# Performance work log

Measured on AMD Instinct MI355X. Metric: run time of the kernel, lower is better.

The kernel has to match this reference:

```python
import jax, jax.numpy as jnp
import numpy as np

B, Q, O = 64, 16, 20   # batch, max questions, max objects
NUM_CAT = 101
D = 256                # category_embedding_dim
T = 4096               # max dialogue length (max_dln)


def setup_inputs() -> dict:
    key = jax.random.key(0)
    k1, k2, k3, k4, k5 = jax.random.split(key, 5)
    object_logits = jax.random.normal(k1, (B, Q, O), dtype=jnp.float32)
    emb_table = jax.random.normal(k2, (NUM_CAT, D), dtype=jnp.float32) * 0.05
    object_categories = jax.random.randint(k3, (B, O), 0, NUM_CAT)
    # sorted, positive cumulative token offsets per (batch, question)
    cumulative_lengths = jnp.sort(jax.random.randint(k4, (B, Q), 1, T + 1), axis=1)
    num_questions = jax.random.randint(k5, (B,), 2, Q + 1)
    return {
        "object_logits": object_logits,
        "emb_table": emb_table,
        "object_categories": object_categories,
        "cumulative_lengths": cumulative_lengths,
        "num_questions": num_questions,
        "max_dln": T,
    }


def reference(object_logits, emb_table, object_categories, cumulative_lengths,
              num_questions, max_dln):
    # --- belief state: softmax -> bmm -> tanh (fused) ---
    probs = jax.nn.softmax(object_logits, axis=-1)          # [B,Q,O]
    obj_emb = emb_table[object_categories]                  # [B,O,D]
    belief = jnp.tanh(jnp.einsum('bqo,bod->bqd', probs, obj_emb))  # [B,Q,D]

    b, q, _ = object_logits.shape
    t = jnp.arange(max_dln)                                 # [T]

    # Ranges in the original loop are contiguous:
    #   qi=0: [0, cum[:,1]-1), qi>=1: [cum[:,qi]-1, cum[:,qi+1]-1)
    # so boundary for question qi's end is cum[:, qi+1]-1 (j = qi+1 in 1..Q-1),
    # valid only for j <= num_questions-1. Mask padded boundaries to +inf.
    j = jnp.arange(1, q)                                    # [Q-1]
    bnd = jnp.where(j[None, :] <= num_questions[:, None] - 1,
                    cumulative_lengths[:, 1:] - 1,
                    max_dln + 1)                            # [B,Q-1]
    # question index owning token t = number of boundaries <= t
    qi = jnp.sum(t[None, None, :] >= bnd[:, :, None], axis=1)  # [B,T] int
    valid = qi < (num_questions[:, None] - 1)               # [B,T]

    qi_c = jnp.minimum(qi, q - 1)
    feats = jnp.take_along_axis(belief, qi_c[:, :, None], axis=1)  # [B,T,D]
    additional_features = jnp.where(valid[:, :, None], feats, 0.0)
    return additional_features
```

## Files before the change

kernel.cpp:

```cpp
#include <hip/hip_runtime.h>
#include <hip/hip_bf16.h>
#include <math.h>

constexpr int B_ = 64;
constexpr int Q_ = 16;
constexpr int O_ = 20;
constexpr int D_ = 256;

__global__ __launch_bounds__(D_) void belief_kernel(
    const float* __restrict__ logits,
    const float* __restrict__ emb,
    const int*   __restrict__ cats,
    float*       __restrict__ belief)
{
    const int bq = blockIdx.x;
    const int b  = bq >> 4;
    const int d  = threadIdx.x;

    __shared__ float s_logit[O_];
    __shared__ int   s_cat[O_];
    if (d < O_) {
        s_logit[d] = logits[bq * O_ + d];
        s_cat[d]   = cats[b * O_ + d];
    }
    __syncthreads();

    float m = -INFINITY;
    #pragma unroll
    for (int o = 0; o < O_; ++o) m = fmaxf(m, s_logit[o]);
    float w[O_];
    float sum = 0.f;
    #pragma unroll
    for (int o = 0; o < O_; ++o) { w[o] = expf(s_logit[o] - m); sum += w[o]; }
    const float inv = 1.f / sum;

    float acc = 0.f;
    #pragma unroll
    for (int o = 0; o < O_; ++o)
        acc = fmaf(w[o] * inv, emb[s_cat[o] * D_ + d], acc);

    belief[bq * D_ + d] = tanhf(acc);
}

constexpr int ROWS_ = 256;

__global__ __launch_bounds__(256) void expand_kernel(
    const float* __restrict__ belief,
    const int*   __restrict__ cum,
    const int*   __restrict__ nq_arr,
    float*       __restrict__ out,
    int T)
{
    const int b   = blockIdx.y;
    const int t0  = blockIdx.x * ROWS_;
    const int tid = threadIdx.x;

    __shared__ float s_belief[Q_ * D_];

    {
        const float4* src = (const float4*)(belief + (size_t)b * Q_ * D_);
        float4*       dst = (float4*)s_belief;
        #pragma unroll
        for (int i = 0; i < (Q_ * D_ / 4) / 256; ++i)
            dst[tid + i * 256] = src[tid + i * 256];
    }

    const int nq = nq_arr[b];
    int bnd[Q_ - 1];
    #pragma unroll
    for (int j = 1; j < Q_; ++j)
        bnd[j - 1] = (j <= nq - 1) ? (cum[b * Q_ + j] - 1) : 0x7fffffff;

    __syncthreads();

    const int col  = (tid & 63) * 4;
    const int rsub = tid >> 6;

    #pragma unroll 4
    for (int it = 0; it < ROWS_ / 4; ++it) {
        const int t = t0 + it * 4 + rsub;
        if (t >= T) break;

        int qi = 0;
        #pragma unroll
        for (int j = 0; j < Q_ - 1; ++j) qi += (t >= bnd[j]) ? 1 : 0;

        float4 v = make_float4(0.f, 0.f, 0.f, 0.f);
        if (qi < nq - 1) {
            const int qc = qi < (Q_ - 1) ? qi : (Q_ - 1);
            v = *(const float4*)(s_belief + qc * D_ + col);
        }
        *(float4*)(out + ((size_t)b * T + t) * (size_t)D_ + col) = v;
    }
}

extern "C" void kernel_launch(void* const* d_in, const int* in_sizes, int n_in,
                              void* d_out, int out_size, void* d_ws, size_t ws_size,
                              hipStream_t stream)
{
    const float* logits = (const float*)d_in[0];
    const float* emb    = (const float*)d_in[1];
    const int*   cats   = (const int*)d_in[2];
    const int*   cum    = (const int*)d_in[3];
    const int*   nq     = (const int*)d_in[4];

    float* out    = (float*)d_out;
    float* belief = (float*)d_ws;

    const int T = out_size / (B_ * D_);

    belief_kernel<<<B_ * Q_, D_, 0, stream>>>(logits, emb, cats, belief);

    dim3 grid((T + ROWS_ - 1) / ROWS_, B_);
    expand_kernel<<<grid, 256, 0, stream>>>(belief, cum, nq, out, T);
}
```

Measured before the change: 270.9 us.

## Fuse belief computation into expand kernel, recomputing per block

Folds the softmax-bmm-tanh belief computation into the expand kernel so each block computes its batch's 16x256 belief tile directly into shared memory. This drops the separate kernel launch and the workspace round trip through global memory. In exchange, every one of the 16 blocks per batch redundantly recomputes the same belief tile, with each thread producing 16 outputs using float4 embedding loads.

```diff
diff --git a/kernel.cpp b/kernel.cpp
--- a/kernel.cpp
+++ b/kernel.cpp
@@ -1,5 +1,4 @@
 #include <hip/hip_runtime.h>
-#include <hip/hip_bf16.h>
 #include <math.h>
 
 constexpr int B_ = 64;
@@ -7,45 +6,12 @@
 constexpr int O_ = 20;
 constexpr int D_ = 256;
 
-__global__ __launch_bounds__(D_) void belief_kernel(
+constexpr int ROWS_ = 256;
+
+__global__ __launch_bounds__(256) void fused_kernel(
     const float* __restrict__ logits,
     const float* __restrict__ emb,
     const int*   __restrict__ cats,
-    float*       __restrict__ belief)
-{
-    const int bq = blockIdx.x;
-    const int b  = bq >> 4;
-    const int d  = threadIdx.x;
-
-    __shared__ float s_logit[O_];
-    __shared__ int   s_cat[O_];
-    if (d < O_) {
-        s_logit[d] = logits[bq * O_ + d];
-        s_cat[d]   = cats[b * O_ + d];
-    }
-    __syncthreads();
-
-    float m = -INFINITY;
-    #pragma unroll
-    for (int o = 0; o < O_; ++o) m = fmaxf(m, s_logit[o]);
-    float w[O_];
-    float sum = 0.f;
-    #pragma unroll
-    for (int o = 0; o < O_; ++o) { w[o] = expf(s_logit[o] - m); sum += w[o]; }
-    const float inv = 1.f / sum;
-
-    float acc = 0.f;
-    #pragma unroll
-    for (int o = 0; o < O_; ++o)
-        acc = fmaf(w[o] * inv, emb[s_cat[o] * D_ + d], acc);
-
-    belief[bq * D_ + d] = tanhf(acc);
-}
-
-constexpr int ROWS_ = 256;
-
-__global__ __launch_bounds__(256) void expand_kernel(
-    const float* __restrict__ belief,
     const int*   __restrict__ cum,
     const int*   __restrict__ nq_arr,
     float*       __restrict__ out,
@@ -56,13 +22,51 @@
     const int tid = threadIdx.x;
 
     __shared__ float s_belief[Q_ * D_];
+    __shared__ float s_logit[Q_ * O_];
+    __shared__ int   s_cat[O_];
+
+    for (int i = tid; i < Q_ * O_; i += 256) s_logit[i] = logits[b * Q_ * O_ + i];
+    if (tid < O_) s_cat[tid] = cats[b * O_ + tid];
+    __syncthreads();
 
     {
-        const float4* src = (const float4*)(belief + (size_t)b * Q_ * D_);
-        float4*       dst = (float4*)s_belief;
+        const int q  = tid >> 4;
+        const int k  = tid & 15;
+        const int d0 = k * 16;
+
+        float m = -INFINITY;
         #pragma unroll
-        for (int i = 0; i < (Q_ * D_ / 4) / 256; ++i)
-            dst[tid + i * 256] = src[tid + i * 256];
+        for (int o = 0; o < O_; ++o) m = fmaxf(m, s_logit[q * O_ + o]);
+        float w[O_];
+        float sum = 0.f;
+        #pragma unroll
+        for (int o = 0; o < O_; ++o) {
+            w[o] = expf(s_logit[q * O_ + o] - m);
+            sum += w[o];
+        }
+        const float inv = 1.f / sum;
+
+        float acc[16];
+        #pragma unroll
+        for (int j = 0; j < 16; ++j) acc[j] = 0.f;
+
+        #pragma unroll
+        for (int o = 0; o < O_; ++o) {
+            const float wo = w[o] * inv;
+            const float4* e = (const float4*)(emb + s_cat[o] * D_ + d0);
+            #pragma unroll
+            for (int j4 = 0; j4 < 4; ++j4) {
+                const float4 v = e[j4];
+                acc[j4 * 4 + 0] = fmaf(wo, v.x, acc[j4 * 4 + 0]);
+                acc[j4 * 4 + 1] = fmaf(wo, v.y, acc[j4 * 4 + 1]);
+                acc[j4 * 4 + 2] = fmaf(wo, v.z, acc[j4 * 4 + 2]);
+                acc[j4 * 4 + 3] = fmaf(wo, v.w, acc[j4 * 4 + 3]);
+            }
+        }
+
+        #pragma unroll
+        for (int j = 0; j < 16; ++j)
+            s_belief[q * D_ + d0 + j] = tanhf(acc[j]);
     }
 
     const int nq = nq_arr[b];
@@ -75,6 +79,7 @@
 
     const int col  = (tid & 63) * 4;
     const int rsub = tid >> 6;
+    float* const out_b = out + (size_t)b * T * (size_t)D_;
 
     #pragma unroll 4
     for (int it = 0; it < ROWS_ / 4; ++it) {
@@ -90,7 +95,7 @@
             const int qc = qi < (Q_ - 1) ? qi : (Q_ - 1);
             v = *(const float4*)(s_belief + qc * D_ + col);
         }
-        *(float4*)(out + ((size_t)b * T + t) * (size_t)D_ + col) = v;
+        *(float4*)(out_b + (size_t)t * D_ + col) = v;
     }
 }
 
@@ -104,13 +109,11 @@
     const int*   cum    = (const int*)d_in[3];
     const int*   nq     = (const int*)d_in[4];
 
-    float* out    = (float*)d_out;
-    float* belief = (float*)d_ws;
-
+    float* out = (float*)d_out;
     const int T = out_size / (B_ * D_);
 
-    belief_kernel<<<B_ * Q_, D_, 0, stream>>>(logits, emb, cats, belief);
+    (void)d_ws; (void)ws_size;
 
     dim3 grid((T + ROWS_ - 1) / ROWS_, B_);
-    expand_kernel<<<grid, 256, 0, stream>>>(belief, cum, nq, out, T);
+    fused_kernel<<<grid, 256, 0, stream>>>(logits, emb, cats, cum, nq, out, T);
 }
```

New measurement: 299.0 us. 1.1x slower.

## Add zero-tail fast path and nontemporal stores in expand kernel

Applied to the files above, without the earlier changes.

The expand kernel now computes the last valid token per batch and lets blocks lying entirely past it write zeros straight away, skipping the shared-memory belief load and the boundary search. All output stores become nontemporal vector stores, and a row's belief vector is reloaded from shared memory only when the question index changes. Rows per block drop from 256 to 128, which gives more blocks and finer-grained early exit. The kernel is bound by writing a large output, so most of the benefit depends on how well nontemporal stores perform compared with normal stores.

```diff
diff --git a/kernel.cpp b/kernel.cpp
--- a/kernel.cpp
+++ b/kernel.cpp
@@ -1,11 +1,12 @@
 #include <hip/hip_runtime.h>
-#include <hip/hip_bf16.h>
 #include <math.h>
 
 constexpr int B_ = 64;
 constexpr int Q_ = 16;
 constexpr int O_ = 20;
 constexpr int D_ = 256;
+
+typedef float vf4 __attribute__((ext_vector_type(4)));
 
 __global__ __launch_bounds__(D_) void belief_kernel(
     const float* __restrict__ logits,
@@ -42,7 +43,7 @@
     belief[bq * D_ + d] = tanhf(acc);
 }
 
-constexpr int ROWS_ = 256;
+constexpr int ROWS_ = 128;
 
 __global__ __launch_bounds__(256) void expand_kernel(
     const float* __restrict__ belief,
@@ -57,15 +58,33 @@
 
     __shared__ float s_belief[Q_ * D_];
 
+    const int nq = nq_arr[b];
+    const int limit = cum[b * Q_ + (nq - 1)] - 1;
+
+    const int col  = (tid & 63) * 4;
+    const int rsub = tid >> 6;
+    float* outp = out + ((size_t)b * T + t0 + rsub) * (size_t)D_ + col;
+
+    if (t0 >= limit) {
+        const vf4 z = {0.f, 0.f, 0.f, 0.f};
+        #pragma unroll 4
+        for (int it = 0; it < ROWS_ / 4; ++it) {
+            const int t = t0 + it * 4 + rsub;
+            if (t >= T) break;
+            __builtin_nontemporal_store(z, (vf4*)outp);
+            outp += 4 * D_;
+        }
+        return;
+    }
+
     {
-        const float4* src = (const float4*)(belief + (size_t)b * Q_ * D_);
-        float4*       dst = (float4*)s_belief;
+        const vf4* src = (const vf4*)(belief + (size_t)b * Q_ * D_);
+        vf4*       dst = (vf4*)s_belief;
         #pragma unroll
         for (int i = 0; i < (Q_ * D_ / 4) / 256; ++i)
             dst[tid + i * 256] = src[tid + i * 256];
     }
 
-    const int nq = nq_arr[b];
     int bnd[Q_ - 1];
     #pragma unroll
     for (int j = 1; j < Q_; ++j)
@@ -73,10 +92,9 @@
 
     __syncthreads();
 
-    const int col  = (tid & 63) * 4;
-    const int rsub = tid >> 6;
+    int prev_r = -2;
+    vf4 v = {0.f, 0.f, 0.f, 0.f};
 
-    #pragma unroll 4
     for (int it = 0; it < ROWS_ / 4; ++it) {
         const int t = t0 + it * 4 + rsub;
         if (t >= T) break;
@@ -84,13 +102,15 @@
         int qi = 0;
         #pragma unroll
         for (int j = 0; j < Q_ - 1; ++j) qi += (t >= bnd[j]) ? 1 : 0;
+        const int r = (qi < nq - 1) ? qi : -1;
 
-        float4 v = make_float4(0.f, 0.f, 0.f, 0.f);
-        if (qi < nq - 1) {
-            const int qc = qi < (Q_ - 1) ? qi : (Q_ - 1);
-            v = *(const float4*)(s_belief + qc * D_ + col);
+        if (r != prev_r) {
+            if (r >= 0) v = *(const vf4*)(s_belief + r * D_ + col);
+            else        v = (vf4){0.f, 0.f, 0.f, 0.f};
+            prev_r = r;
         }
-        *(float4*)(out + ((size_t)b * T + t) * (size_t)D_ + col) = v;
+        __builtin_nontemporal_store(v, (vf4*)outp);
+        outp += 4 * D_;
     }
 }
 
@@ -106,7 +126,6 @@
 
     float* out    = (float*)d_out;
     float* belief = (float*)d_ws;
-
     const int T = out_size / (B_ * D_);
 
     belief_kernel<<<B_ * Q_, D_, 0, stream>>>(logits, emb, cats, belief);
```

Measured after the change: 286.1 us. +5.6%, slower.
